# Optimization experiments

Measured on AMD Instinct MI355X. Metric: run time of the kernel, lower is better.

The kernel has to match this reference:

```python
import jax, jax.numpy as jnp
import numpy as np
import math

B, S, D = 4, 1024, 1024
H = 16
NQ = 8
HEAD_DIM = D // H
ALPHA = 0.7


def setup_inputs() -> dict:
    key = jax.random.key(0)
    ks = jax.random.split(key, 11)
    s = 1.0 / math.sqrt(D)
    return {
        "query": jax.random.normal(ks[0], (B, S, D), jnp.float32),
        "key": jax.random.normal(ks[1], (B, S, D), jnp.float32),
        "value": jax.random.normal(ks[2], (B, S, D), jnp.float32),
        "Wq": jax.random.normal(ks[3], (D, D), jnp.float32) * s,
        "bq": jnp.zeros((D,), jnp.float32),
        "Wk": jax.random.normal(ks[4], (D, D), jnp.float32) * s,
        "bk": jnp.zeros((D,), jnp.float32),
        "Wv": jax.random.normal(ks[5], (D, D), jnp.float32) * s,
        "bv": jnp.zeros((D,), jnp.float32),
        "Wo": jax.random.normal(ks[6], (D, D), jnp.float32) * s,
        "bo": jnp.zeros((D,), jnp.float32),
    }


def _pairwise_entropy(query, key):
    # tanh-encode and take first NQ features: [B, S, NQ]
    q_enc = jnp.tanh(query)[:, :, :NQ]
    k_enc = jnp.tanh(key)[:, :, :NQ]
    # combined[b,i,j,:] = concat(q_enc[b,i], k_enc[b,j]) -> [B, S, S, 2*NQ]
    qi = jnp.broadcast_to(q_enc[:, :, None, :], (B, S, S, NQ))
    kj = jnp.broadcast_to(k_enc[:, None, :, :], (B, S, S, NQ))
    combined = jnp.concatenate([qi, kj], axis=-1)
    probs = jax.nn.softmax(combined, axis=-1)
    # von Neumann-style entropy with the module's 1e-8 epsilon
    entropy = -jnp.sum(probs * jnp.log(probs + 1e-8), axis=-1)  # [B, S, S]
    return entropy


def reference(query, key, value, Wq, bq, Wk, bk, Wv, bv, Wo, bo):
    # Linear projections (torch Linear: x @ W^T + b)
    Q = query @ Wq.T + bq
    K = key @ Wk.T + bk
    V = value @ Wv.T + bv
    # [B, H, S, head_dim]
    Qh = Q.reshape(B, S, H, HEAD_DIM).transpose(0, 2, 1, 3)
    Kh = K.reshape(B, S, H, HEAD_DIM).transpose(0, 2, 1, 3)
    Vh = V.reshape(B, S, H, HEAD_DIM).transpose(0, 2, 1, 3)
    classical = jnp.einsum('bhsd,bhtd->bhst', Qh, Kh) / math.sqrt(HEAD_DIM)
    quantum = _pairwise_entropy(query, key)  # [B, S, S]
    combined = ALPHA * classical.mean(axis=1) + (1.0 - ALPHA) * quantum
    attn = jax.nn.softmax(combined, axis=-1)  # [B, S, S]
    # shared attention across heads
    attended = jnp.einsum('bst,bhtd->bhsd', attn, Vh)
    attended = attended.transpose(0, 2, 1, 3).reshape(B, S, D)
    output = attended @ Wo.T + bo
    return output, attn
```

## Files before the change

### kernel.cpp

```cpp
#include <hip/hip_runtime.h>


typedef float f32x4 __attribute__((ext_vector_type(4)));
typedef short s16x8 __attribute__((ext_vector_type(8)));
typedef unsigned short u16;

#define Bc 4
#define Sc 1024
#define Dc 1024
#define NTOK (Bc * Sc)
#define CSCALE (0.7f / 128.0f)
#define ESCALE 0.3f

typedef void __attribute__((address_space(1))) as1_void;
typedef void __attribute__((address_space(3))) as3_void;

__device__ __forceinline__ u16 f2b(float f) {
  union { float f; unsigned u; } v; v.f = f;
  unsigned r = v.u + 0x7fffu + ((v.u >> 16) & 1u);
  return (u16)(r >> 16);
}

__device__ __forceinline__ void xcd_map(int& bx, int& by, int& bz) {
  const int gx = gridDim.x, gy = gridDim.y;
  const int nwg = gx * gy * gridDim.z;
  const int lid = blockIdx.x + gx * (blockIdx.y + gy * blockIdx.z);
  const int cpx = nwg >> 3;
  const int s = (lid & 7) * cpx + (lid >> 3);
  bx = s % gx; const int r = s / gx; by = r % gy; bz = r / gy;
}

__global__ __launch_bounds__(256) void cast_bf16(const float* __restrict__ in,
                                                 u16* __restrict__ out, int n4) {
  int i = blockIdx.x * 256 + threadIdx.x;
  if (i >= n4) return;
  float4 v = reinterpret_cast<const float4*>(in)[i];
  ushort4 o = make_ushort4(f2b(v.x), f2b(v.y), f2b(v.z), f2b(v.w));
  reinterpret_cast<ushort4*>(out)[i] = o;
}

__global__ __launch_bounds__(256) void ent_agg(const float* __restrict__ q,
                                               const float* __restrict__ k,
                                               float* __restrict__ agg) {
  int r = blockIdx.x * 256 + threadIdx.x;
  if (r >= 2 * NTOK) return;
  const float* src = (r < NTOK) ? (q + (size_t)r * Dc) : (k + (size_t)(r - NTOK) * Dc);
  float A = 0.f, Sv = 0.f;
#pragma unroll
  for (int m = 0; m < 8; ++m) {
    float e = tanhf(src[m]);
    float a = __expf(e);
    A += a; Sv += a * e;
  }
  if (r < NTOK) { agg[r] = A; agg[NTOK + r] = Sv; }
  else          { agg[NTOK + r] = A; agg[3 * NTOK + (r - NTOK)] = Sv; }
}

template<int BM>
__device__ __forceinline__ void gemm2(const u16* __restrict__ A, const u16* __restrict__ Bt,
                                      int K, int row0, int col0,
                                      f32x4 (*acc)[4]) {
  constexpr int MR = BM / 32;
  __shared__ __align__(16) u16 LA[2][BM * 32];
  __shared__ __align__(16) u16 LB[2][128 * 32];
  const int tid = threadIdx.x;
  const int lane = tid & 63, wave = tid >> 6;
  const int wr = wave >> 1, wc = wave & 1;
  const int fr = lane & 15, g = lane >> 4;

  const int rA0 = tid >> 2;
  const int slA0 = (tid & 3) ^ ((rA0 >> 1) & 3);
  const u16* gA0 = A + (size_t)(row0 + rA0) * K + slA0 * 8;
  const u16* gA1 = nullptr;
  if constexpr (BM == 128) {
    const int rA1 = rA0 + 64;
    const int slA1 = (tid & 3) ^ ((rA1 >> 1) & 3);
    gA1 = A + (size_t)(row0 + rA1) * K + slA1 * 8;
  }
  const int rB1 = rA0 + 64;
  const int slB1 = (tid & 3) ^ ((rB1 >> 1) & 3);
  const u16* gB0 = Bt + (size_t)(col0 + rA0) * K + slA0 * 8;
  const u16* gB1 = Bt + (size_t)(col0 + rB1) * K + slB1 * 8;

  int aoff[MR], boff[4];
#pragma unroll
  for (int i = 0; i < MR; ++i) {
    const int row = wr * (MR * 16) + i * 16 + fr;
    aoff[i] = row * 32 + ((g ^ ((row >> 1) & 3)) << 3);
  }
#pragma unroll
  for (int j = 0; j < 4; ++j) {
    const int row = wc * 64 + j * 16 + fr;
    boff[j] = row * 32 + ((g ^ ((row >> 1) & 3)) << 3);
  }

  auto stage = [&](int buf, int kt) {
    const int ko = kt * 32;
    __builtin_amdgcn_global_load_lds((const as1_void*)(gA0 + ko),
                                     (as3_void*)(&LA[buf][tid * 8]), 16, 0, 0);
    if constexpr (BM == 128)
      __builtin_amdgcn_global_load_lds((const as1_void*)(gA1 + ko),
                                       (as3_void*)(&LA[buf][(256 + tid) * 8]), 16, 0, 0);
    __builtin_amdgcn_global_load_lds((const as1_void*)(gB0 + ko),
                                     (as3_void*)(&LB[buf][tid * 8]), 16, 0, 0);
    __builtin_amdgcn_global_load_lds((const as1_void*)(gB1 + ko),
                                     (as3_void*)(&LB[buf][(256 + tid) * 8]), 16, 0, 0);
  };

  const int nk = K >> 5;
  stage(0, 0);
  asm volatile("s_waitcnt vmcnt(0)" ::: "memory");
  __builtin_amdgcn_s_barrier();
  __builtin_amdgcn_sched_barrier(0);

  for (int kt = 0; kt < nk; ++kt) {
    const int cur = kt & 1;
    if (kt + 1 < nk) stage(cur ^ 1, kt + 1);
    s16x8 af[MR], bf[4];
#pragma unroll
    for (int i = 0; i < MR; ++i) af[i] = *reinterpret_cast<const s16x8*>(&LA[cur][aoff[i]]);
#pragma unroll
    for (int j = 0; j < 4; ++j) bf[j] = *reinterpret_cast<const s16x8*>(&LB[cur][boff[j]]);
#pragma unroll
    for (int i = 0; i < MR; ++i)
#pragma unroll
      for (int j = 0; j < 4; ++j)
        acc[i][j] = __builtin_amdgcn_mfma_f32_16x16x32_bf16(af[i], bf[j], acc[i][j], 0, 0, 0);
    if (kt + 1 < nk) {
      asm volatile("s_waitcnt vmcnt(0)" ::: "memory");
      __builtin_amdgcn_s_barrier();
      __builtin_amdgcn_sched_barrier(0);
    }
  }
}

__global__ __launch_bounds__(256, 4) void gemm_proj(const u16* __restrict__ Xall,
                                                    const u16* __restrict__ Wall,
                                                    const float* __restrict__ biasq,
                                                    const float* __restrict__ biask,
                                                    const float* __restrict__ biasv,
                                                    u16* __restrict__ QKout,
                                                    u16* __restrict__ Vt) {
  int bx, by, z; xcd_map(bx, by, z);
  const int row0 = bx * 128, col0 = by * 128;
  const u16* A  = Xall + (size_t)z * NTOK * Dc;
  const u16* Bt = Wall + (size_t)z * Dc * Dc;
  f32x4 acc[4][4] = {};
  gemm2<128>(A, Bt, Dc, row0, col0, acc);

  const int lane = threadIdx.x & 63, wave = threadIdx.x >> 6;
  const int wm = (wave >> 1) * 64, wn = (wave & 1) * 64;
  const int cr = (lane >> 4) * 4, cc = lane & 15;
  const float* bias = (z == 0) ? biasq : (z == 1) ? biask : biasv;
#pragma unroll
  for (int j = 0; j < 4; ++j) {
    const int gc = col0 + wn + j * 16 + cc;
    const float bb = bias[gc];
#pragma unroll
    for (int i = 0; i < 4; ++i) {
      const int gr = row0 + wm + i * 16 + cr;
      f32x4 v = acc[i][j];
      if (z < 2) {
        u16* dst = QKout + (size_t)z * NTOK * Dc + (size_t)gr * Dc + gc;
#pragma unroll
        for (int r = 0; r < 4; ++r) dst[(size_t)r * Dc] = f2b(v[r] + bb);
      } else {
        const int b = gr >> 10, t = gr & (Sc - 1);
        ushort4 o = make_ushort4(f2b(v[0] + bb), f2b(v[1] + bb), f2b(v[2] + bb), f2b(v[3] + bb));
        *reinterpret_cast<ushort4*>(Vt + (size_t)b * Dc * Sc + (size_t)gc * Sc + t) = o;
      }
    }
  }
}

__global__ __launch_bounds__(256, 4) void gemm_scores(const u16* __restrict__ Qb,
                                                      const u16* __restrict__ Kb,
                                                      const float* __restrict__ agg,
                                                      float* __restrict__ comb) {
  int bx, by, z; xcd_map(bx, by, z);
  const int row0 = bx * 64, col0 = by * 128;
  const u16* A  = Qb + (size_t)z * Sc * Dc;
  const u16* Bt = Kb + (size_t)z * Sc * Dc;
  f32x4 acc[2][4] = {};
  gemm2<64>(A, Bt, Dc, row0, col0, acc);

  const int lane = threadIdx.x & 63, wave = threadIdx.x >> 6;
  const int wm = (wave >> 1) * 32, wn = (wave & 1) * 64;
  const int cr = (lane >> 4) * 4, cc = lane & 15;
  const float* qA = agg + (size_t)z * Sc;
  const float* qS = agg + NTOK + (size_t)z * Sc;
  const float* kA = agg + 2 * NTOK + (size_t)z * Sc;
  const float* kS = agg + 3 * NTOK + (size_t)z * Sc;
  float* C = comb + (size_t)z * Sc * Sc;
#pragma unroll
  for (int j = 0; j < 4; ++j) {
    const int gc = col0 + wn + j * 16 + cc;
    const float kAv = kA[gc], kSv = kS[gc];
#pragma unroll
    for (int i = 0; i < 2; ++i) {
      const int gr = row0 + wm + i * 16 + cr;
      f32x4 v = acc[i][j];
#pragma unroll
      for (int r = 0; r < 4; ++r) {
        const int s = gr + r;
        const float Z = qA[s] + kAv;
        const float ent = __logf(Z) - (qS[s] + kSv) / Z;
        C[(size_t)s * Sc + gc] = CSCALE * v[r] + ESCALE * ent;
      }
    }
  }
}

__global__ __launch_bounds__(256) void softmax_row(const float* __restrict__ comb,
                                                   float* __restrict__ attn_f,
                                                   u16* __restrict__ attn_b) {
  const int row = blockIdx.x;
  const int t = threadIdx.x;
  const float* src = comb + (size_t)row * Sc;
  float4 v = reinterpret_cast<const float4*>(src)[t];
  float m = fmaxf(fmaxf(v.x, v.y), fmaxf(v.z, v.w));
#pragma unroll
  for (int off = 1; off < 64; off <<= 1) m = fmaxf(m, __shfl_xor(m, off));
  __shared__ float red[8];
  if ((t & 63) == 0) red[t >> 6] = m;
  __syncthreads();
  m = fmaxf(fmaxf(red[0], red[1]), fmaxf(red[2], red[3]));
  float e0 = __expf(v.x - m), e1 = __expf(v.y - m), e2 = __expf(v.z - m), e3 = __expf(v.w - m);
  float s = e0 + e1 + e2 + e3;
#pragma unroll
  for (int off = 1; off < 64; off <<= 1) s += __shfl_xor(s, off);
  if ((t & 63) == 0) red[4 + (t >> 6)] = s;
  __syncthreads();
  s = red[4] + red[5] + red[6] + red[7];
  const float inv = 1.f / s;
  float4 o = make_float4(e0 * inv, e1 * inv, e2 * inv, e3 * inv);
  reinterpret_cast<float4*>(attn_f + (size_t)row * Sc)[t] = o;
  ushort4 ob = make_ushort4(f2b(o.x), f2b(o.y), f2b(o.z), f2b(o.w));
  reinterpret_cast<ushort4*>(attn_b + (size_t)row * Sc)[t] = ob;
}

__global__ __launch_bounds__(256, 4) void gemm_av(const u16* __restrict__ attnb,
                                                  const u16* __restrict__ Vt,
                                                  u16* __restrict__ att) {
  int bx, by, z; xcd_map(bx, by, z);
  const int row0 = bx * 64, col0 = by * 128;
  const u16* A  = attnb + (size_t)z * Sc * Sc;
  const u16* Bt = Vt + (size_t)z * Dc * Sc;
  f32x4 acc[2][4] = {};
  gemm2<64>(A, Bt, Sc, row0, col0, acc);

  const int lane = threadIdx.x & 63, wave = threadIdx.x >> 6;
  const int wm = (wave >> 1) * 32, wn = (wave & 1) * 64;
  const int cr = (lane >> 4) * 4, cc = lane & 15;
  u16* C = att + (size_t)z * Sc * Dc;
#pragma unroll
  for (int j = 0; j < 4; ++j) {
    const int gc = col0 + wn + j * 16 + cc;
#pragma unroll
    for (int i = 0; i < 2; ++i) {
      const int gr = row0 + wm + i * 16 + cr;
      f32x4 v = acc[i][j];
#pragma unroll
      for (int r = 0; r < 4; ++r) C[(size_t)(gr + r) * Dc + gc] = f2b(v[r]);
    }
  }
}

__global__ __launch_bounds__(256, 4) void gemm_out(const u16* __restrict__ att,
                                                   const u16* __restrict__ Wob,
                                                   const float* __restrict__ bo,
                                                   float* __restrict__ out) {
  int bx, by, bz; xcd_map(bx, by, bz);
  const int row0 = bx * 64, col0 = by * 128;
  f32x4 acc[2][4] = {};
  gemm2<64>(att, Wob, Dc, row0, col0, acc);

  const int lane = threadIdx.x & 63, wave = threadIdx.x >> 6;
  const int wm = (wave >> 1) * 32, wn = (wave & 1) * 64;
  const int cr = (lane >> 4) * 4, cc = lane & 15;
#pragma unroll
  for (int j = 0; j < 4; ++j) {
    const int gc = col0 + wn + j * 16 + cc;
    const float bb = bo[gc];
#pragma unroll
    for (int i = 0; i < 2; ++i) {
      const int gr = row0 + wm + i * 16 + cr;
      f32x4 v = acc[i][j];
#pragma unroll
      for (int r = 0; r < 4; ++r) out[(size_t)(gr + r) * Dc + gc] = v[r] + bb;
    }
  }
}

extern "C" void kernel_launch(void* const* d_in, const int* in_sizes, int n_in,
                              void* d_out, int out_size, void* d_ws, size_t ws_size,
                              hipStream_t stream) {
  const float* query = (const float*)d_in[0];
  const float* key   = (const float*)d_in[1];
  const float* value = (const float*)d_in[2];
  const float* Wq = (const float*)d_in[3];
  const float* bq = (const float*)d_in[4];
  const float* Wk = (const float*)d_in[5];
  const float* bk = (const float*)d_in[6];
  const float* Wv = (const float*)d_in[7];
  const float* bv = (const float*)d_in[8];
  const float* Wo = (const float*)d_in[9];
  const float* bo = (const float*)d_in[10];

  float* out    = (float*)d_out;
  float* attn_f = out + (size_t)NTOK * Dc;

  char* w = (char*)d_ws;
  const size_t MB = 1ull << 20;
  u16* qx = (u16*)(w);
  u16* kx = (u16*)(w + 8 * MB);
  u16* vx = (u16*)(w + 16 * MB);
  float* comb = (float*)(w);
  u16* attnb  = (u16*)(w + 16 * MB);
  u16* Qb = (u16*)(w + 24 * MB);
  u16* attended = (u16*)(w + 24 * MB);
  u16* Vt = (u16*)(w + 40 * MB);
  u16* Wb = (u16*)(w + 48 * MB);
  float* agg = (float*)(w + 56 * MB);

  const int n4tok = NTOK * Dc / 4;
  const int n4w   = Dc * Dc / 4;

  cast_bf16<<<n4tok / 256, 256, 0, stream>>>(query, qx, n4tok);
  cast_bf16<<<n4tok / 256, 256, 0, stream>>>(key,   kx, n4tok);
  cast_bf16<<<n4tok / 256, 256, 0, stream>>>(value, vx, n4tok);
  cast_bf16<<<n4w / 256, 256, 0, stream>>>(Wq, Wb + 0ull * Dc * Dc, n4w);
  cast_bf16<<<n4w / 256, 256, 0, stream>>>(Wk, Wb + 1ull * Dc * Dc, n4w);
  cast_bf16<<<n4w / 256, 256, 0, stream>>>(Wv, Wb + 2ull * Dc * Dc, n4w);
  cast_bf16<<<n4w / 256, 256, 0, stream>>>(Wo, Wb + 3ull * Dc * Dc, n4w);

  ent_agg<<<(2 * NTOK) / 256, 256, 0, stream>>>(query, key, agg);

  gemm_proj<<<dim3(32, 8, 3), 256, 0, stream>>>(qx, Wb, bq, bk, bv, Qb, Vt);

  gemm_scores<<<dim3(16, 8, 4), 256, 0, stream>>>(Qb, Qb + (size_t)NTOK * Dc, agg, comb);

  softmax_row<<<NTOK, 256, 0, stream>>>(comb, attn_f, attnb);

  gemm_av<<<dim3(16, 8, 4), 256, 0, stream>>>(attnb, Vt, attended);

  gemm_out<<<dim3(64, 8, 1), 256, 0, stream>>>(attended, Wb + 3ull * Dc * Dc, bo, out);

  (void)in_sizes; (void)n_in; (void)out_size; (void)ws_size;
}
```

Baseline: 245.7 us.

## Triple-buffer GEMM LDS pipeline and merge seven cast launches into one

The shared GEMM mainloop goes from double to triple buffering. It prefetches two K-tiles ahead and waits only on the older tile's loads through partial vmcnt counts, instead of draining every load before each barrier. The seven separate fp32-to-bf16 cast launches become one kernel that picks source and destination by thread index, cutting launch overhead. The extra LDS buffer lowers occupancy, and gemm_proj's launch bounds drop to 3 blocks per CU. K is now hardcoded to 1024.

```diff
diff --git a/kernel.cpp b/kernel.cpp
--- a/kernel.cpp
+++ b/kernel.cpp
@@ -30,13 +30,29 @@
   bx = s % gx; const int r = s / gx; by = r % gy; bz = r / gy;
 }
 
-__global__ __launch_bounds__(256) void cast_bf16(const float* __restrict__ in,
-                                                 u16* __restrict__ out, int n4) {
-  int i = blockIdx.x * 256 + threadIdx.x;
-  if (i >= n4) return;
-  float4 v = reinterpret_cast<const float4*>(in)[i];
-  ushort4 o = make_ushort4(f2b(v.x), f2b(v.y), f2b(v.z), f2b(v.w));
-  reinterpret_cast<ushort4*>(out)[i] = o;
+__global__ __launch_bounds__(256) void cast_all(const float* __restrict__ q,
+                                                const float* __restrict__ k,
+                                                const float* __restrict__ v,
+                                                const float* __restrict__ wq,
+                                                const float* __restrict__ wk,
+                                                const float* __restrict__ wv,
+                                                const float* __restrict__ wo,
+                                                u16* __restrict__ qx, u16* __restrict__ kx,
+                                                u16* __restrict__ vx, u16* __restrict__ Wb) {
+  const int i = blockIdx.x * 256 + threadIdx.x;
+  const float* src; u16* dst; int off;
+  if (i < 3145728) {
+    const int t = i >> 20; off = i & 1048575;
+    src = (t == 0) ? q : (t == 1) ? k : v;
+    dst = (t == 0) ? qx : (t == 1) ? kx : vx;
+  } else {
+    const int j = i - 3145728; const int t = j >> 18; off = j & 262143;
+    src = (t == 0) ? wq : (t == 1) ? wk : (t == 2) ? wv : wo;
+    dst = Wb + (size_t)t * Dc * Dc;
+  }
+  float4 vv = reinterpret_cast<const float4*>(src)[off];
+  reinterpret_cast<ushort4*>(dst)[off] =
+      make_ushort4(f2b(vv.x), f2b(vv.y), f2b(vv.z), f2b(vv.w));
 }
 
 __global__ __launch_bounds__(256) void ent_agg(const float* __restrict__ q,
@@ -56,13 +72,15 @@
   else          { agg[NTOK + r] = A; agg[3 * NTOK + (r - NTOK)] = Sv; }
 }
 
-template<int BM>
-__device__ __forceinline__ void gemm2(const u16* __restrict__ A, const u16* __restrict__ Bt,
-                                      int K, int row0, int col0,
-                                      f32x4 (*acc)[4]) {
+template<int BM, int NL>
+__device__ __forceinline__ void gemm3(const u16* __restrict__ A, const u16* __restrict__ Bt,
+                                      int row0, int col0, f32x4 (*acc)[4]) {
   constexpr int MR = BM / 32;
-  __shared__ __align__(16) u16 LA[2][BM * 32];
-  __shared__ __align__(16) u16 LB[2][128 * 32];
+  constexpr int ASZ = BM * 32;
+  constexpr int BSZ = 128 * 32;
+  constexpr int K = 1024, nk = 32;
+  __shared__ __align__(16) u16 LA[3 * ASZ];
+  __shared__ __align__(16) u16 LB[3 * BSZ];
   const int tid = threadIdx.x;
   const int lane = tid & 63, wave = tid >> 6;
   const int wr = wave >> 1, wc = wave & 1;
@@ -94,47 +112,56 @@
     boff[j] = row * 32 + ((g ^ ((row >> 1) & 3)) << 3);
   }
 
-  auto stage = [&](int buf, int kt) {
+  auto stage = [&](int aofs, int bofs, int kt) {
     const int ko = kt * 32;
     __builtin_amdgcn_global_load_lds((const as1_void*)(gA0 + ko),
-                                     (as3_void*)(&LA[buf][tid * 8]), 16, 0, 0);
+                                     (as3_void*)(&LA[aofs + tid * 8]), 16, 0, 0);
     if constexpr (BM == 128)
       __builtin_amdgcn_global_load_lds((const as1_void*)(gA1 + ko),
-                                       (as3_void*)(&LA[buf][(256 + tid) * 8]), 16, 0, 0);
+                                       (as3_void*)(&LA[aofs + (256 + tid) * 8]), 16, 0, 0);
     __builtin_amdgcn_global_load_lds((const as1_void*)(gB0 + ko),
-                                     (as3_void*)(&LB[buf][tid * 8]), 16, 0, 0);
+                                     (as3_void*)(&LB[bofs + tid * 8]), 16, 0, 0);
     __builtin_amdgcn_global_load_lds((const as1_void*)(gB1 + ko),
-                                     (as3_void*)(&LB[buf][(256 + tid) * 8]), 16, 0, 0);
+                                     (as3_void*)(&LB[bofs + (256 + tid) * 8]), 16, 0, 0);
   };
 
-  const int nk = K >> 5;
-  stage(0, 0);
-  asm volatile("s_waitcnt vmcnt(0)" ::: "memory");
+  stage(0, 0, 0);
+  stage(ASZ, BSZ, 1);
+  if constexpr (NL == 4) asm volatile("s_waitcnt vmcnt(4)" ::: "memory");
+  else                   asm volatile("s_waitcnt vmcnt(3)" ::: "memory");
   __builtin_amdgcn_s_barrier();
   __builtin_amdgcn_sched_barrier(0);
 
+  int a0 = 0, a1 = ASZ, a2 = 2 * ASZ;
+  int b0 = 0, b1 = BSZ, b2 = 2 * BSZ;
   for (int kt = 0; kt < nk; ++kt) {
-    const int cur = kt & 1;
-    if (kt + 1 < nk) stage(cur ^ 1, kt + 1);
+    if (kt + 2 < nk) stage(a2, b2, kt + 2);
     s16x8 af[MR], bf[4];
 #pragma unroll
-    for (int i = 0; i < MR; ++i) af[i] = *reinterpret_cast<const s16x8*>(&LA[cur][aoff[i]]);
-#pragma unroll
-    for (int j = 0; j < 4; ++j) bf[j] = *reinterpret_cast<const s16x8*>(&LB[cur][boff[j]]);
+    for (int i = 0; i < MR; ++i) af[i] = *reinterpret_cast<const s16x8*>(&LA[a0 + aoff[i]]);
+#pragma unroll
+    for (int j = 0; j < 4; ++j) bf[j] = *reinterpret_cast<const s16x8*>(&LB[b0 + boff[j]]);
 #pragma unroll
     for (int i = 0; i < MR; ++i)
 #pragma unroll
       for (int j = 0; j < 4; ++j)
         acc[i][j] = __builtin_amdgcn_mfma_f32_16x16x32_bf16(af[i], bf[j], acc[i][j], 0, 0, 0);
     if (kt + 1 < nk) {
-      asm volatile("s_waitcnt vmcnt(0)" ::: "memory");
+      if (kt + 2 < nk) {
+        if constexpr (NL == 4) asm volatile("s_waitcnt vmcnt(4)" ::: "memory");
+        else                   asm volatile("s_waitcnt vmcnt(3)" ::: "memory");
+      } else {
+        asm volatile("s_waitcnt vmcnt(0)" ::: "memory");
+      }
       __builtin_amdgcn_s_barrier();
       __builtin_amdgcn_sched_barrier(0);
     }
-  }
-}
-
-__global__ __launch_bounds__(256, 4) void gemm_proj(const u16* __restrict__ Xall,
+    int t = a0; a0 = a1; a1 = a2; a2 = t;
+    t = b0; b0 = b1; b1 = b2; b2 = t;
+  }
+}
+
+__global__ __launch_bounds__(256, 3) void gemm_proj(const u16* __restrict__ Xall,
                                                     const u16* __restrict__ Wall,
                                                     const float* __restrict__ biasq,
                                                     const float* __restrict__ biask,
@@ -146,7 +173,7 @@
   const u16* A  = Xall + (size_t)z * NTOK * Dc;
   const u16* Bt = Wall + (size_t)z * Dc * Dc;
   f32x4 acc[4][4] = {};
-  gemm2<128>(A, Bt, Dc, row0, col0, acc);
+  gemm3<128, 4>(A, Bt, row0, col0, acc);
 
   const int lane = threadIdx.x & 63, wave = threadIdx.x >> 6;
   const int wm = (wave >> 1) * 64, wn = (wave & 1) * 64;
@@ -182,7 +209,7 @@
   const u16* A  = Qb + (size_t)z * Sc * Dc;
   const u16* Bt = Kb + (size_t)z * Sc * Dc;
   f32x4 acc[2][4] = {};
-  gemm2<64>(A, Bt, Dc, row0, col0, acc);
+  gemm3<64, 3>(A, Bt, row0, col0, acc);
 
   const int lane = threadIdx.x & 63, wave = threadIdx.x >> 6;
   const int wm = (wave >> 1) * 32, wn = (wave & 1) * 64;
@@ -247,7 +274,7 @@
   const u16* A  = attnb + (size_t)z * Sc * Sc;
   const u16* Bt = Vt + (size_t)z * Dc * Sc;
   f32x4 acc[2][4] = {};
-  gemm2<64>(A, Bt, Sc, row0, col0, acc);
+  gemm3<64, 3>(A, Bt, row0, col0, acc);
 
   const int lane = threadIdx.x & 63, wave = threadIdx.x >> 6;
   const int wm = (wave >> 1) * 32, wn = (wave & 1) * 64;
@@ -273,7 +300,7 @@
   int bx, by, bz; xcd_map(bx, by, bz);
   const int row0 = bx * 64, col0 = by * 128;
   f32x4 acc[2][4] = {};
-  gemm2<64>(att, Wob, Dc, row0, col0, acc);
+  gemm3<64, 3>(att, Wob, row0, col0, acc);
 
   const int lane = threadIdx.x & 63, wave = threadIdx.x >> 6;
   const int wm = (wave >> 1) * 32, wn = (wave & 1) * 64;
@@ -323,16 +350,7 @@
   u16* Wb = (u16*)(w + 48 * MB);
   float* agg = (float*)(w + 56 * MB);
 
-  const int n4tok = NTOK * Dc / 4;
-  const int n4w   = Dc * Dc / 4;
-
-  cast_bf16<<<n4tok / 256, 256, 0, stream>>>(query, qx, n4tok);
-  cast_bf16<<<n4tok / 256, 256, 0, stream>>>(key,   kx, n4tok);
-  cast_bf16<<<n4tok / 256, 256, 0, stream>>>(value, vx, n4tok);
-  cast_bf16<<<n4w / 256, 256, 0, stream>>>(Wq, Wb + 0ull * Dc * Dc, n4w);
-  cast_bf16<<<n4w / 256, 256, 0, stream>>>(Wk, Wb + 1ull * Dc * Dc, n4w);
-  cast_bf16<<<n4w / 256, 256, 0, stream>>>(Wv, Wb + 2ull * Dc * Dc, n4w);
-  cast_bf16<<<n4w / 256, 256, 0, stream>>>(Wo, Wb + 3ull * Dc * Dc, n4w);
+  cast_all<<<16384, 256, 0, stream>>>(query, key, value, Wq, Wk, Wv, Wo, qx, kx, vx, Wb);
 
   ent_agg<<<(2 * NTOK) / 256, 256, 0, stream>>>(query, key, agg);
 
```

Result: faster. 233.6 us (-4.9%).
